# Performance work log

Hardware: AMD Instinct MI355X
Metric: run time of the kernel (lower is better)

The kernel has to match this reference:

```python
import jax, jax.numpy as jnp
import numpy as np
from jax import lax

B = 32; C_IN = 3; HW = 64
CL1_F = 64; CL1_K = 5
V = 1024
CL2_F = 128; CL2_K = 16
CL3_F = 256; CL3_K = 16
FC1_F = 512; FC2_F = 10
FC1_IN = CL3_F * (V // 16)  # 16384


def _sym_laplacian(k, v):
    # symmetric, spectral norm < 1 (mimics rescaled Laplacian 2L/lmax - I spectrum)
    a = jax.random.normal(k, (v, v), jnp.float32) / np.float32(np.sqrt(v))
    return (a + a.T) * jnp.float32(0.3)


def setup_inputs():
    key = jax.random.key(0)
    ks = jax.random.split(key, 10)
    def n(k, shape, s):
        return jax.random.normal(k, shape, jnp.float32) * jnp.float32(s)
    x = jax.random.normal(ks[0], (B, C_IN, HW, HW), jnp.float32)
    conv1_w = n(ks[1], (CL1_F, C_IN, CL1_K, CL1_K), 0.05)
    conv1_b = jnp.zeros((CL1_F,), jnp.float32)
    L1 = _sym_laplacian(ks[2], V)
    L2 = _sym_laplacian(ks[3], V // 4)
    g = HW // 2  # pooled grid side = 32
    ii, jj = jnp.meshgrid(jnp.arange(g), jnp.arange(g), indexing='ij')
    node_index = jnp.stack([ii.reshape(-1), jj.reshape(-1)], axis=1).astype(jnp.int32)  # [V,2]
    perm = jnp.arange(V, dtype=jnp.int32)
    k2_w = n(ks[4], (CL2_F, CL1_F * CL2_K), 0.04)
    k2_b = jnp.zeros((CL2_F,), jnp.float32)
    k3_w = n(ks[5], (CL3_F, CL2_F * CL3_K), 0.03)
    k3_b = jnp.zeros((CL3_F,), jnp.float32)
    fc1_w = n(ks[6], (FC1_F, FC1_IN), 0.01)
    fc1_b = jnp.zeros((FC1_F,), jnp.float32)
    fc2_w = n(ks[7], (FC2_F, FC1_F), 0.05)
    fc2_b = jnp.zeros((FC2_F,), jnp.float32)
    return {"x": x, "conv1_w": conv1_w, "conv1_b": conv1_b, "L1": L1, "L2": L2,
            "node_index": node_index, "perm": perm,
            "k2_w": k2_w, "k2_b": k2_b, "k3_w": k3_w, "k3_b": k3_b,
            "fc1_w": fc1_w, "fc1_b": fc1_b, "fc2_w": fc2_w, "fc2_b": fc2_b}


def _graph_conv(x, L, W, b, K):
    # x: (B, C, V). Chebyshev basis T_k(L) x, then linear over (C*K).
    Bb, C, Vv = x.shape
    x0 = jnp.transpose(x, (2, 1, 0)).reshape(Vv, C * Bb)  # [V, C*B]
    xs = [x0, L @ x0]
    for _ in range(K - 2):
        xs.append(2.0 * (L @ xs[-1]) - xs[-2])
    xk = jnp.stack(xs, axis=0).reshape(K, Vv, C, Bb)  # [K,V,C,B]
    xk = jnp.transpose(xk, (3, 1, 2, 0)).reshape(Bb * Vv, C * K)  # [B*V, C*K]
    out = xk @ W.T + b  # [B*V, Fout]
    return jnp.transpose(out.reshape(Bb, Vv, -1), (0, 2, 1))  # (B, Fout, V)


def reference(x, conv1_w, conv1_b, L1, L2, node_index, perm,
              k2_w, k2_b, k3_w, k3_b, fc1_w, fc1_b, fc2_w, fc2_b):
    pad = (CL1_K - 1) // 2
    y = lax.conv_general_dilated(x, conv1_w, (1, 1), [(pad, pad), (pad, pad)],
                                 dimension_numbers=('NCHW', 'OIHW', 'NCHW'))
    y = jax.nn.relu(y + conv1_b[None, :, None, None])
    Bb, C, H, Wd = y.shape
    y = y.reshape(Bb, C, H // 2, 2, Wd // 2, 2).max(axis=(3, 5))  # MaxPool2d(2,2)
    y = y[:, :, node_index[:, 0], node_index[:, 1]]  # (B, C, V)
    y = y[:, :, perm]
    # BatchNorm1d(affine=False), training-mode batch stats, biased variance
    mean = y.mean(axis=(0, 2), keepdims=True)
    var = y.var(axis=(0, 2), keepdims=True)
    y = (y - mean) * lax.rsqrt(var + 1e-5)
    y = jax.nn.relu(_graph_conv(y, L1, k2_w, k2_b, CL2_K))
    y = y.reshape(Bb, CL2_F, -1, 4).max(axis=-1)  # Graph_MaxPool(4)
    y = jax.nn.relu(_graph_conv(y, L2, k3_w, k3_b, CL3_K))
    y = y.reshape(Bb, CL3_F, -1, 4).max(axis=-1)
    y = y.reshape(Bb, FC1_IN)
    y = jax.nn.relu(y @ fc1_w.T + fc1_b)  # dropout p=0 -> identity
    return y @ fc2_w.T + fc2_b
```

## Files before the change

### kernel.cpp

```cpp
#include <hip/hip_runtime.h>
#include <hip/hip_bf16.h>

#define BB 32
#define C_IN 3
#define HW 64
#define V1 1024
#define CL2_F 128
#define V2 256
#define CL3_F 256
#define FC1_IN 16384

typedef unsigned short ushortT;
typedef __attribute__((ext_vector_type(8))) short bf16x8;
typedef __attribute__((ext_vector_type(8))) unsigned short u16x8;
typedef __attribute__((ext_vector_type(4))) float f32x4;

__device__ __forceinline__ float bfu2f(unsigned short u) {
  union { unsigned int i; float f; } x; x.i = ((unsigned)u) << 16; return x.f;
}
__device__ __forceinline__ unsigned short f2bf(float v) {
  union { float f; unsigned int i; } x; x.f = v;
  unsigned r = x.i + 0x7FFFu + ((x.i >> 16) & 1u);
  return (unsigned short)(r >> 16);
}
__device__ __forceinline__ void gload16(const ushortT* g, ushortT* l) {
  __builtin_amdgcn_global_load_lds((const __attribute__((address_space(1))) void*)g,
                                   (__attribute__((address_space(3))) void*)l, 16, 0, 0);
}

__global__ __launch_bounds__(256) void conv_pool_k(const float* __restrict__ x,
                                                   const float* __restrict__ w,
                                                   const float* __restrict__ bias,
                                                   float* __restrict__ P) {
  __shared__ float xs[3][7][72];
  __shared__ float wl[64][76];
  const int b = blockIdx.x >> 5, ph = blockIdx.x & 31;
  const int t = threadIdx.x;
  for (int i = t; i < 64 * 75; i += 256) wl[i / 75][i % 75] = w[i];
  for (int i = t; i < 3 * 7 * 72; i += 256) {
    int col = i % 72, rr = (i / 72) % 7, ci = i / (72 * 7);
    int ih = 2 * ph - 2 + rr, iw = col - 2;
    float v = 0.f;
    if (ih >= 0 && ih < HW && iw >= 0 && iw < HW)
      v = x[((b * 3 + ci) * HW + ih) * HW + iw];
    xs[ci][rr][col] = v;
  }
  __syncthreads();
  const int co = t >> 2, pq = t & 3;
  float acc[8][2][2];
#pragma unroll
  for (int i = 0; i < 8; ++i)
#pragma unroll
    for (int a = 0; a < 2; ++a)
#pragma unroll
      for (int d = 0; d < 2; ++d) acc[i][a][d] = 0.f;
  for (int ci = 0; ci < 3; ++ci) {
#pragma unroll
    for (int kh = 0; kh < 5; ++kh) {
      float w5[5];
#pragma unroll
      for (int j = 0; j < 5; ++j) w5[j] = wl[co][ci * 25 + kh * 5 + j];
#pragma unroll
      for (int dy = 0; dy < 2; ++dy) {
        const int r = kh + dy;
        float in[20];
#pragma unroll
        for (int q4 = 0; q4 < 5; ++q4) {
          float4 v4 = *(const float4*)&xs[ci][r][16 * pq + q4 * 4];
          in[q4 * 4 + 0] = v4.x; in[q4 * 4 + 1] = v4.y;
          in[q4 * 4 + 2] = v4.z; in[q4 * 4 + 3] = v4.w;
        }
#pragma unroll
        for (int i = 0; i < 8; ++i)
#pragma unroll
          for (int dx = 0; dx < 2; ++dx)
#pragma unroll
            for (int kw = 0; kw < 5; ++kw)
              acc[i][dy][dx] += w5[kw] * in[2 * i + dx + kw];
      }
    }
  }
  const float bv = bias[co];
#pragma unroll
  for (int i = 0; i < 8; ++i) {
    float m = fmaxf(fmaxf(acc[i][0][0], acc[i][0][1]), fmaxf(acc[i][1][0], acc[i][1][1]));
    P[((size_t)(b * 64 + co) << 10) + (ph << 5) + pq * 8 + i] = fmaxf(m + bv, 0.f);
  }
}

__global__ __launch_bounds__(256) void bn_part_k(const float* __restrict__ P,
                                                 float* __restrict__ buf) {
  int c = blockIdx.x, s = blockIdx.y;
  float s1 = 0.f, s2 = 0.f;
  for (int i = threadIdx.x; i < 4096; i += 256) {
    int b = s * 4 + (i >> 10), p = i & 1023;
    float v = P[((size_t)(b * 64 + c) << 10) + p];
    s1 += v; s2 += v * v;
  }
#pragma unroll
  for (int o = 32; o > 0; o >>= 1) { s1 += __shfl_down(s1, o); s2 += __shfl_down(s2, o); }
  __shared__ float sh[2][4];
  int wid = threadIdx.x >> 6;
  if ((threadIdx.x & 63) == 0) { sh[0][wid] = s1; sh[1][wid] = s2; }
  __syncthreads();
  if (threadIdx.x == 0) {
    buf[c * 8 + s] = sh[0][0] + sh[0][1] + sh[0][2] + sh[0][3];
    buf[512 + c * 8 + s] = sh[1][0] + sh[1][1] + sh[1][2] + sh[1][3];
  }
}
__global__ __launch_bounds__(64) void bn_comb_k(float* __restrict__ buf) {
  int c = threadIdx.x;
  float s1 = 0.f, s2 = 0.f;
#pragma unroll
  for (int s = 0; s < 8; ++s) { s1 += buf[c * 8 + s]; s2 += buf[512 + c * 8 + s]; }
  float mean = s1 / 32768.f;
  float var = s2 / 32768.f - mean * mean;
  buf[1024 + c] = mean;
  buf[1088 + c] = rsqrtf(var + 1e-5f);
}

__global__ __launch_bounds__(256) void build_x0_k(const float* __restrict__ P,
                                                  const float* __restrict__ buf,
                                                  const int* __restrict__ ni,
                                                  const int* __restrict__ perm,
                                                  ushortT* __restrict__ PGh,
                                                  ushortT* __restrict__ PGl,
                                                  ushortT* __restrict__ CW0) {
  __shared__ float vals[64][33];
  __shared__ int qv[32];
  const int b = blockIdx.x >> 5, vc = blockIdx.x & 31;
  const int t = threadIdx.x;
  if (t < 32) {
    int pv = perm[vc * 32 + t];
    qv[t] = ni[2 * pv] * 32 + ni[2 * pv + 1];
  }
  __syncthreads();
  {
    int c = t & 63, vh = t >> 6;
    float mean = buf[1024 + c], rstd = buf[1088 + c];
    const float* pc = &P[((size_t)(b * 64 + c)) << 10];
#pragma unroll
    for (int j = 0; j < 8; ++j) {
      int vl = vh * 8 + j;
      vals[c][vl] = (pc[qv[vl]] - mean) * rstd;
    }
  }
  __syncthreads();
  {
    int c = t & 63, vo = t >> 6;
    u16x8 h8, l8;
#pragma unroll
    for (int j = 0; j < 8; ++j) {
      float f = vals[c][vo * 8 + j];
      unsigned short h = f2bf(f);
      h8[j] = h; l8[j] = f2bf(f - bfu2f(h));
    }
    size_t base = ((size_t)(vc * 4 + vo) * 2048 + b * 64 + c) * 8;
    *(u16x8*)&PGh[base] = h8;
    *(u16x8*)&PGl[base] = l8;
  }
  {
    int co = t & 7, vl = t >> 3;
    u16x8 h8;
#pragma unroll
    for (int j = 0; j < 8; ++j) h8[j] = f2bf(vals[co * 8 + j][vl]);
    *(u16x8*)&CW0[((size_t)co * 32768 + b * 1024 + vc * 32 + vl) * 8] = h8;
  }
}

__global__ __launch_bounds__(256) void lsplit_k(const float* __restrict__ L,
                                                ushortT* __restrict__ Lh,
                                                ushortT* __restrict__ Ll, int V) {
  int id = blockIdx.x * 256 + threadIdx.x;
  int n = id & (V - 1), koct = id / V * 8;
  u16x8 h8, l8;
#pragma unroll
  for (int j = 0; j < 8; ++j) {
    float v = L[(size_t)(koct + j) * V + n];
    unsigned short h = f2bf(v);
    h8[j] = h; l8[j] = f2bf(v - bfu2f(h));
  }
  size_t o = (size_t)id * 8;
  *(u16x8*)&Lh[o] = h8;
  *(u16x8*)&Ll[o] = l8;
}

__global__ __launch_bounds__(256) void wprep_k(const float* __restrict__ W,
                                               ushortT* __restrict__ WAh,
                                               ushortT* __restrict__ WAl, int Cc, int Nf) {
  int d = blockIdx.x * 256 + threadIdx.x;
  if (d >= Nf * 16 * Cc) return;
  int c = d % Cc, kq = (d / Cc) % 16, f = d / (16 * Cc);
  float v = W[(size_t)f * (Cc * 16) + c * 16 + kq];
  unsigned short h = f2bf(v);
  WAh[d] = h; WAl[d] = f2bf(v - bfu2f(h));
}

template <int MODE, int SWZ>
__global__ __launch_bounds__(256, 2) void cheb_step_k(
    int Mld, int Kd, int mt,
    const ushortT* __restrict__ Ah, const ushortT* __restrict__ Al,
    const ushortT* __restrict__ Lbh, const ushortT* __restrict__ Lbl,
    ushortT* __restrict__ Ph, ushortT* __restrict__ Pl,
    ushortT* __restrict__ CW, int CB, int CSH) {
  __shared__ ushortT sA[2][2][8][520];
  __shared__ ushortT sB[2][2][8][520];
  int bx, by;
  if (SWZ) {
    const int id = blockIdx.x;
    const int xcd = id & 7, pos = id >> 3;
    bx = (xcd & 3) * 8 + (pos & 7);
    by = (xcd >> 2) * 8 + (pos >> 3);
  } else {
    bx = blockIdx.x % mt;
    by = blockIdx.x / mt;
  }
  const int m0 = bx * 64, n0 = by * 64;
  const int t = threadIdx.x, lane = t & 63;
  const int wr = (t >> 6) >> 1, wc = (t >> 6) & 1;
  const int lm = lane & 15, lq = lane >> 4;

  f32x4 acc[2][2];
#pragma unroll
  for (int mi = 0; mi < 2; ++mi)
#pragma unroll
    for (int nj = 0; nj < 2; ++nj) acc[mi][nj] = (f32x4){0.f, 0.f, 0.f, 0.f};

#define STAGEK(buf, k0)                                                            \
  {                                                                                \
    const int koct = (k0) >> 3;                                                    \
    _Pragma("unroll") for (int i = 0; i < 2; ++i) {                                \
      const int slot = (t + i * 256) >> 6;                                         \
      const int ln = t & 63;                                                       \
      const size_t ga = ((size_t)(koct + slot) * Mld + m0 + ln) * 8;               \
      const size_t gb = ((size_t)(koct + slot) * Kd + n0 + ln) * 8;                \
      gload16(Ah + ga, &sA[buf][0][slot][0]);                                      \
      gload16(Al + ga, &sA[buf][1][slot][0]);                                      \
      gload16(Lbh + gb, &sB[buf][0][slot][0]);                                     \
      gload16(Lbl + gb, &sB[buf][1][slot][0]);                                     \
    }                                                                              \
  }

  STAGEK(0, 0);
  __syncthreads();
  for (int k0 = 0; k0 < Kd; k0 += 64) {
    const int cur = (k0 >> 6) & 1;
    if (k0 + 64 < Kd) STAGEK(cur ^ 1, k0 + 64);
#pragma unroll
    for (int ks = 0; ks < 2; ++ks) {
      const int so = ks * 4 + lq;
      bf16x8 xah[2], xal[2], xbh[2], xbl[2];
#pragma unroll
      for (int mi = 0; mi < 2; ++mi) {
        const int r = (wr * 32 + mi * 16 + lm) * 8;
        xah[mi] = *(const bf16x8*)&sA[cur][0][so][r];
        xal[mi] = *(const bf16x8*)&sA[cur][1][so][r];
      }
#pragma unroll
      for (int nj = 0; nj < 2; ++nj) {
        const int r = (wc * 32 + nj * 16 + lm) * 8;
        xbh[nj] = *(const bf16x8*)&sB[cur][0][so][r];
        xbl[nj] = *(const bf16x8*)&sB[cur][1][so][r];
      }
#pragma unroll
      for (int mi = 0; mi < 2; ++mi)
#pragma unroll
        for (int nj = 0; nj < 2; ++nj) {
          acc[mi][nj] = __builtin_amdgcn_mfma_f32_16x16x32_bf16(xah[mi], xbh[nj], acc[mi][nj], 0, 0, 0);
          acc[mi][nj] = __builtin_amdgcn_mfma_f32_16x16x32_bf16(xal[mi], xbh[nj], acc[mi][nj], 0, 0, 0);
          acc[mi][nj] = __builtin_amdgcn_mfma_f32_16x16x32_bf16(xah[mi], xbl[nj], acc[mi][nj], 0, 0, 0);
        }
    }
    __syncthreads();
  }
#undef STAGEK

  float* fs = (float*)&sA[0][0][0][0];
#pragma unroll
  for (int mi = 0; mi < 2; ++mi)
#pragma unroll
    for (int nj = 0; nj < 2; ++nj)
#pragma unroll
      for (int j = 0; j < 4; ++j) {
        int gm_l = wr * 32 + mi * 16 + lq * 4 + j;
        int gn_l = wc * 32 + nj * 16 + lm;
        fs[gm_l * 65 + gn_l] = acc[mi][nj][j];
      }
  __syncthreads();

  const size_t noct0 = (size_t)(n0 >> 3);
#pragma unroll
  for (int r = 0; r < 2; ++r) {
    int id = t + r * 256;
    int gm_l = id >> 3, go = id & 7;
    size_t g = ((noct0 + go) * Mld + (m0 + gm_l)) * 8;
    float nv[8];
#pragma unroll
    for (int i = 0; i < 8; ++i) nv[i] = fs[gm_l * 65 + go * 8 + i];
    if (MODE == 1) {
      u16x8 ph = *(const u16x8*)&Ph[g];
      u16x8 pl = *(const u16x8*)&Pl[g];
#pragma unroll
      for (int i = 0; i < 8; ++i) nv[i] = 2.f * nv[i] - (bfu2f(ph[i]) + bfu2f(pl[i]));
    }
    u16x8 h8, l8;
#pragma unroll
    for (int i = 0; i < 8; ++i) {
      unsigned short h = f2bf(nv[i]);
      h8[i] = h; l8[i] = f2bf(nv[i] - bfu2f(h));
    }
    *(u16x8*)&Ph[g] = h8;
    *(u16x8*)&Pl[g] = l8;
    if (MODE == 1) {
#pragma unroll
      for (int i = 0; i < 8; ++i) fs[gm_l * 65 + go * 8 + i] = nv[i];
    }
  }
  __syncthreads();

  const int cBase = m0 & (CB - 1);
  const int bidx = m0 >> CSH;
  const size_t NNs = (size_t)Kd << 5;
#pragma unroll
  for (int r = 0; r < 2; ++r) {
    int id = t + r * 256;
    int gn_l = id & 63, coI = id >> 6;
    u16x8 h8;
#pragma unroll
    for (int i = 0; i < 8; ++i) h8[i] = f2bf(fs[(coI * 8 + i) * 65 + gn_l]);
    size_t cbase = ((size_t)((cBase >> 3) + coI) * NNs + (size_t)bidx * Kd + n0 + gn_l) * 8;
    *(u16x8*)&CW[cbase] = h8;
  }
}

template <int Cc>
__global__ __launch_bounds__(256) void wapply_k(
    int NN, int ldw,
    const ushortT* __restrict__ WAh, const ushortT* __restrict__ WAl,
    const ushortT* __restrict__ cwBase, size_t cwN,
    float* __restrict__ OUT) {
  constexpr int S = Cc / 2;
  const int m0 = blockIdx.x * 64, n0 = blockIdx.y * 128;
  const int t = threadIdx.x, lane = t & 63, wid = t >> 6;
  const int wr = wid >> 1, wc = wid & 1;
  const int lm = lane & 15, lq = lane >> 4;

  const size_t wBase = (size_t)(m0 + wr * 32 + lm) * ldw + lq * 8;
  const int nb = n0 + wc * 64 + lm;

  f32x4 acc[2][4];
#pragma unroll
  for (int mi = 0; mi < 2; ++mi)
#pragma unroll
    for (int nj = 0; nj < 4; ++nj) acc[mi][nj] = (f32x4){0.f, 0.f, 0.f, 0.f};

#pragma unroll 4
  for (int s = 0; s < S; ++s) {
    const int buf = (Cc == 64) ? (s >> 1) : (s >> 2);
    const int lo = (Cc == 64) ? ((s & 1) * 4) : ((s & 3) * 4);
    const ushortT* xb = cwBase + (size_t)buf * cwN;
    bf16x8 wh[2], wl[2], xf[4];
#pragma unroll
    for (int mi = 0; mi < 2; ++mi) {
      size_t o = wBase + (size_t)s * 32 + (size_t)mi * 16 * ldw;
      wh[mi] = *(const bf16x8*)(WAh + o);
      wl[mi] = *(const bf16x8*)(WAl + o);
    }
#pragma unroll
    for (int nj = 0; nj < 4; ++nj)
      xf[nj] = *(const bf16x8*)(xb + ((size_t)(lo + lq) * NN + nb + nj * 16) * 8);
#pragma unroll
    for (int mi = 0; mi < 2; ++mi)
#pragma unroll
      for (int nj = 0; nj < 4; ++nj) {
        acc[mi][nj] = __builtin_amdgcn_mfma_f32_16x16x32_bf16(wh[mi], xf[nj], acc[mi][nj], 0, 0, 0);
        acc[mi][nj] = __builtin_amdgcn_mfma_f32_16x16x32_bf16(wl[mi], xf[nj], acc[mi][nj], 0, 0, 0);
      }
  }

#pragma unroll
  for (int mi = 0; mi < 2; ++mi)
#pragma unroll
    for (int nj = 0; nj < 4; ++nj)
#pragma unroll
      for (int j = 0; j < 4; ++j) {
        int gm = m0 + wr * 32 + mi * 16 + lq * 4 + j;
        int gn = n0 + wc * 64 + nj * 16 + lm;
        OUT[(size_t)gm * NN + gn] = acc[mi][nj][j];
      }
}

__global__ __launch_bounds__(256) void relu_pool1_k(const float* __restrict__ OUT1T,
                                                    const float* __restrict__ b2,
                                                    ushortT* __restrict__ PG2h,
                                                    ushortT* __restrict__ PG2l,
                                                    ushortT* __restrict__ CW0) {
  __shared__ float sval[128][9];
  const int b = blockIdx.x >> 5, vc = blockIdx.x & 31;
  const int t = threadIdx.x;
  {
    int f = t & 127, h = t >> 7;
    float bb = b2[f];
    const float* src = &OUT1T[(size_t)f * 32768 + b * 1024 + vc * 32];
#pragma unroll
    for (int i = 0; i < 4; ++i) {
      int v2l = h * 4 + i;
      float4 r = *(const float4*)&src[v2l * 4];
      float m = fmaxf(fmaxf(r.x, r.y), fmaxf(r.z, r.w));
      sval[f][v2l] = fmaxf(m + bb, 0.f);
    }
  }
  __syncthreads();
  if (t < 128) {
    int f = t;
    u16x8 h8, l8;
#pragma unroll
    for (int j = 0; j < 8; ++j) {
      float v = sval[f][j];
      unsigned short h = f2bf(v);
      h8[j] = h; l8[j] = f2bf(v - bfu2f(h));
    }
    size_t base = ((size_t)vc * 4096 + b * 128 + f) * 8;
    *(u16x8*)&PG2h[base] = h8;
    *(u16x8*)&PG2l[base] = l8;
  } else {
    int q = t - 128;
    int co = q & 15, v2l = q >> 4;
    u16x8 h8;
#pragma unroll
    for (int j = 0; j < 8; ++j) h8[j] = f2bf(sval[co * 8 + j][v2l]);
    *(u16x8*)&CW0[((size_t)co * 8192 + b * 256 + vc * 8 + v2l) * 8] = h8;
  }
}

__global__ __launch_bounds__(256) void relu_pool2_k(const float* __restrict__ OUT2T,
                                                    const float* __restrict__ b3,
                                                    float* __restrict__ At) {
  int n = blockIdx.x * 256 + threadIdx.x;
  int v3 = n & 63, f = (n >> 6) & 255, b = n >> 14;
  float4 r = *(const float4*)&OUT2T[((size_t)f * 32 + b) * 256 + v3 * 4];
  float m = fmaxf(fmaxf(r.x, r.y), fmaxf(r.z, r.w));
  At[(size_t)b * FC1_IN + f * 64 + v3] = fmaxf(m + b3[f], 0.f);
}

__global__ __launch_bounds__(256) void fc1_part_k(const float* __restrict__ At,
                                                  const float* __restrict__ W1,
                                                  float* __restrict__ part) {
  __shared__ float sWt[64][68];
  __shared__ float sA[64][33];
  const int jt = blockIdx.x, ks = blockIdx.y;
  const int j0 = jt * 64, kb = ks * 512;
  const int t = threadIdx.x;
  const int b = t & 31, jg = t >> 5;
  float acc[8] = {};
  for (int k0 = kb; k0 < kb + 512; k0 += 64) {
    __syncthreads();
    {
      int jr = t >> 2, kq = t & 3;
      const float* wp = &W1[(size_t)(j0 + jr) * FC1_IN + k0 + kq * 16];
#pragma unroll
      for (int i = 0; i < 4; ++i) {
        float4 w4 = *(const float4*)(wp + 4 * i);
        int kk = kq * 16 + 4 * i;
        sWt[kk + 0][jr] = w4.x; sWt[kk + 1][jr] = w4.y;
        sWt[kk + 2][jr] = w4.z; sWt[kk + 3][jr] = w4.w;
      }
    }
    {
      int br = t >> 3, ko = t & 7;
      const float* ap = &At[(size_t)br * FC1_IN + k0 + ko * 8];
      float4 a0 = *(const float4*)ap;
      float4 a1 = *(const float4*)(ap + 4);
      int kk = ko * 8;
      sA[kk + 0][br] = a0.x; sA[kk + 1][br] = a0.y; sA[kk + 2][br] = a0.z; sA[kk + 3][br] = a0.w;
      sA[kk + 4][br] = a1.x; sA[kk + 5][br] = a1.y; sA[kk + 6][br] = a1.z; sA[kk + 7][br] = a1.w;
    }
    __syncthreads();
#pragma unroll 8
    for (int kk = 0; kk < 64; ++kk) {
      float a = sA[kk][b];
      float wv[8];
      *(float4*)wv = *(const float4*)&sWt[kk][jg * 8];
      *(float4*)(wv + 4) = *(const float4*)&sWt[kk][jg * 8 + 4];
#pragma unroll
      for (int i = 0; i < 8; ++i) acc[i] += wv[i] * a;
    }
  }
#pragma unroll
  for (int i = 0; i < 8; ++i)
    part[((size_t)ks * 512 + j0 + jg * 8 + i) * 32 + b] = acc[i];
}

__global__ __launch_bounds__(256) void fc1_combine_k(const float* __restrict__ part,
                                                     const float* __restrict__ b1,
                                                     float* __restrict__ h) {
  int n = blockIdx.x * 256 + threadIdx.x;
  int b = n >> 9, j = n & 511;
  float s = b1[j];
#pragma unroll
  for (int ks = 0; ks < 32; ++ks) s += part[((size_t)ks * 512 + j) * 32 + b];
  h[n] = fmaxf(s, 0.f);
}

__global__ __launch_bounds__(64) void fc2_k(const float* __restrict__ h,
                                            const float* __restrict__ W2,
                                            const float* __restrict__ b2f,
                                            float* __restrict__ out) {
  int n = blockIdx.x * 64 + threadIdx.x;
  if (n >= 320) return;
  int b = n / 10, o = n % 10;
  float s = b2f[o];
  const float* hp = h + b * 512;
  const float* wp = W2 + o * 512;
  for (int j = 0; j < 512; ++j) s += hp[j] * wp[j];
  out[n] = s;
}

extern "C" void kernel_launch(void* const* d_in, const int* in_sizes, int n_in,
                              void* d_out, int out_size, void* d_ws, size_t ws_size,
                              hipStream_t stream) {
  const float* x      = (const float*)d_in[0];
  const float* conv1w = (const float*)d_in[1];
  const float* conv1b = (const float*)d_in[2];
  const float* L1     = (const float*)d_in[3];
  const float* L2     = (const float*)d_in[4];
  const int*   ni     = (const int*)d_in[5];
  const int*   perm   = (const int*)d_in[6];
  const float* k2w    = (const float*)d_in[7];
  const float* k2b    = (const float*)d_in[8];
  const float* k3w    = (const float*)d_in[9];
  const float* k3b    = (const float*)d_in[10];
  const float* fc1w   = (const float*)d_in[11];
  const float* fc1b   = (const float*)d_in[12];
  const float* fc2w   = (const float*)d_in[13];
  const float* fc2b   = (const float*)d_in[14];
  float* out = (float*)d_out;

  char* ws = (char*)d_ws;
  const size_t MB = 1024 * 1024;
  float*   P    = (float*)(ws + 0);
  ushortT* cw1  = (ushortT*)(ws + 8 * MB);
  const size_t CW1N = 2u * 1024 * 1024;
  ushortT* pgAh = (ushortT*)(ws + 72 * MB);
  ushortT* pgAl = (ushortT*)(ws + 76 * MB);
  ushortT* pgBh = (ushortT*)(ws + 80 * MB);
  ushortT* pgBl = (ushortT*)(ws + 84 * MB);
  float*   OUT1T = (float*)(ws + 88 * MB);
  ushortT* L1h  = (ushortT*)(ws + 105 * MB);
  ushortT* L1l  = (ushortT*)(ws + 107 * MB);
  ushortT* WA1h = (ushortT*)(ws + 109 * MB);
  ushortT* WA1l = (ushortT*)(ws + 109 * MB + 262144);
  float*   BNB  = (float*)(ws + 110 * MB);
  ushortT* cw2  = (ushortT*)(ws + 0);
  const size_t CW2N = 1024u * 1024;
  ushortT* pg2Ah = (ushortT*)(ws + 32 * MB);
  ushortT* pg2Al = (ushortT*)(ws + 34 * MB);
  ushortT* pg2Bh = (ushortT*)(ws + 36 * MB);
  ushortT* pg2Bl = (ushortT*)(ws + 38 * MB);
  float*   OUT2T = (float*)(ws + 40 * MB);
  ushortT* L2h  = (ushortT*)(ws + 48 * MB);
  ushortT* L2l  = (ushortT*)(ws + 48 * MB + 131072);
  ushortT* WA2h = (ushortT*)(ws + 49 * MB);
  ushortT* WA2l = (ushortT*)(ws + 50 * MB);
  float*   At   = (float*)(ws + 51 * MB);
  float*   PART = (float*)(ws + 53 * MB);
  float*   H    = (float*)(ws + 55 * MB);

  conv_pool_k<<<1024, 256, 0, stream>>>(x, conv1w, conv1b, P);
  bn_part_k<<<dim3(64, 8), 256, 0, stream>>>(P, BNB);
  bn_comb_k<<<1, 64, 0, stream>>>(BNB);
  lsplit_k<<<512, 256, 0, stream>>>(L1, L1h, L1l, 1024);
  wprep_k<<<512, 256, 0, stream>>>(k2w, WA1h, WA1l, 64, 128);
  build_x0_k<<<1024, 256, 0, stream>>>(P, BNB, ni, perm, pgAh, pgAl, cw1 + 0 * CW1N);

  cheb_step_k<0, 1><<<512, 256, 0, stream>>>(2048, 1024, 32, pgAh, pgAl, L1h, L1l,
                                             pgBh, pgBl, cw1 + 1 * CW1N, 64, 6);
  for (int k = 2; k < 16; ++k) {
    ushortT *ah, *al, *oh, *ol;
    if (k & 1) { ah = pgAh; al = pgAl; oh = pgBh; ol = pgBl; }
    else       { ah = pgBh; al = pgBl; oh = pgAh; ol = pgAl; }
    cheb_step_k<1, 1><<<512, 256, 0, stream>>>(2048, 1024, 32, ah, al, L1h, L1l,
                                               oh, ol, cw1 + (size_t)k * CW1N, 64, 6);
  }
  wapply_k<64><<<dim3(2, 256), 256, 0, stream>>>(32768, 1024, WA1h, WA1l, cw1, CW1N, OUT1T);

  relu_pool1_k<<<1024, 256, 0, stream>>>(OUT1T, k2b, pg2Ah, pg2Al, cw2 + 0 * CW2N);
  lsplit_k<<<32, 256, 0, stream>>>(L2, L2h, L2l, 256);
  wprep_k<<<2048, 256, 0, stream>>>(k3w, WA2h, WA2l, 128, 256);

  cheb_step_k<0, 0><<<256, 256, 0, stream>>>(4096, 256, 64, pg2Ah, pg2Al, L2h, L2l,
                                             pg2Bh, pg2Bl, cw2 + 1 * CW2N, 128, 7);
  for (int k = 2; k < 16; ++k) {
    ushortT *ah, *al, *oh, *ol;
    if (k & 1) { ah = pg2Ah; al = pg2Al; oh = pg2Bh; ol = pg2Bl; }
    else       { ah = pg2Bh; al = pg2Bl; oh = pg2Ah; ol = pg2Al; }
    cheb_step_k<1, 0><<<256, 256, 0, stream>>>(4096, 256, 64, ah, al, L2h, L2l,
                                               oh, ol, cw2 + (size_t)k * CW2N, 128, 7);
  }
  wapply_k<128><<<dim3(4, 64), 256, 0, stream>>>(8192, 2048, WA2h, WA2l, cw2, CW2N, OUT2T);

  relu_pool2_k<<<2048, 256, 0, stream>>>(OUT2T, k3b, At);
  fc1_part_k<<<dim3(8, 32), 256, 0, stream>>>(At, fc1w, PART);
  fc1_combine_k<<<64, 256, 0, stream>>>(PART, fc1b, H);
  fc2_k<<<5, 64, 0, stream>>>(H, fc2w, fc2b, out);
}
```

Before: 606.4 us.

## Split-K the weight-apply GEMMs and read Laplacian operands directly from global

The weight-apply kernels now split their reduction dimension across a grid z-dimension, 2 slices for stage 1 and 4 for stage 2. Each slice writes its own partial output buffer, and the relu/pool kernels sum the partials before the max. This raises the block count to fill more CUs, at the cost of extra partial-buffer traffic and a relocated workspace layout. Separately, the Chebyshev step kernel no longer stages the Laplacian tile in LDS. Each wave loads its B fragments straight from global into registers, halving shared memory but relying on cache hits for reuse across waves.

```diff
diff --git a/kernel.cpp b/kernel.cpp
--- a/kernel.cpp
+++ b/kernel.cpp
@@ -204,7 +204,6 @@
     ushortT* __restrict__ Ph, ushortT* __restrict__ Pl,
     ushortT* __restrict__ CW, int CB, int CSH) {
   __shared__ ushortT sA[2][2][8][520];
-  __shared__ ushortT sB[2][2][8][520];
   int bx, by;
   if (SWZ) {
     const int id = blockIdx.x;
@@ -219,6 +218,7 @@
   const int t = threadIdx.x, lane = t & 63;
   const int wr = (t >> 6) >> 1, wc = (t >> 6) & 1;
   const int lm = lane & 15, lq = lane >> 4;
+  const size_t bCol = (size_t)(n0 + wc * 32 + lm);
 
   f32x4 acc[2][2];
 #pragma unroll
@@ -226,30 +226,36 @@
 #pragma unroll
     for (int nj = 0; nj < 2; ++nj) acc[mi][nj] = (f32x4){0.f, 0.f, 0.f, 0.f};
 
-#define STAGEK(buf, k0)                                                            \
+#define STAGEA(buf, k0)                                                            \
   {                                                                                \
     const int koct = (k0) >> 3;                                                    \
     _Pragma("unroll") for (int i = 0; i < 2; ++i) {                                \
       const int slot = (t + i * 256) >> 6;                                         \
       const int ln = t & 63;                                                       \
       const size_t ga = ((size_t)(koct + slot) * Mld + m0 + ln) * 8;               \
-      const size_t gb = ((size_t)(koct + slot) * Kd + n0 + ln) * 8;                \
       gload16(Ah + ga, &sA[buf][0][slot][0]);                                      \
       gload16(Al + ga, &sA[buf][1][slot][0]);                                      \
-      gload16(Lbh + gb, &sB[buf][0][slot][0]);                                     \
-      gload16(Lbl + gb, &sB[buf][1][slot][0]);                                     \
     }                                                                              \
   }
 
-  STAGEK(0, 0);
+  STAGEA(0, 0);
   __syncthreads();
   for (int k0 = 0; k0 < Kd; k0 += 64) {
     const int cur = (k0 >> 6) & 1;
-    if (k0 + 64 < Kd) STAGEK(cur ^ 1, k0 + 64);
+    if (k0 + 64 < Kd) STAGEA(cur ^ 1, k0 + 64);
+    bf16x8 xbh[2][2], xbl[2][2];
+#pragma unroll
+    for (int ks = 0; ks < 2; ++ks)
+#pragma unroll
+      for (int nj = 0; nj < 2; ++nj) {
+        size_t o = ((size_t)((k0 >> 3) + ks * 4 + lq) * Kd + bCol + nj * 16) * 8;
+        xbh[ks][nj] = *(const bf16x8*)(Lbh + o);
+        xbl[ks][nj] = *(const bf16x8*)(Lbl + o);
+      }
 #pragma unroll
     for (int ks = 0; ks < 2; ++ks) {
       const int so = ks * 4 + lq;
-      bf16x8 xah[2], xal[2], xbh[2], xbl[2];
+      bf16x8 xah[2], xal[2];
 #pragma unroll
       for (int mi = 0; mi < 2; ++mi) {
         const int r = (wr * 32 + mi * 16 + lm) * 8;
@@ -257,23 +263,17 @@
         xal[mi] = *(const bf16x8*)&sA[cur][1][so][r];
       }
 #pragma unroll
-      for (int nj = 0; nj < 2; ++nj) {
-        const int r = (wc * 32 + nj * 16 + lm) * 8;
-        xbh[nj] = *(const bf16x8*)&sB[cur][0][so][r];
-        xbl[nj] = *(const bf16x8*)&sB[cur][1][so][r];
-      }
-#pragma unroll
       for (int mi = 0; mi < 2; ++mi)
 #pragma unroll
         for (int nj = 0; nj < 2; ++nj) {
-          acc[mi][nj] = __builtin_amdgcn_mfma_f32_16x16x32_bf16(xah[mi], xbh[nj], acc[mi][nj], 0, 0, 0);
-          acc[mi][nj] = __builtin_amdgcn_mfma_f32_16x16x32_bf16(xal[mi], xbh[nj], acc[mi][nj], 0, 0, 0);
-          acc[mi][nj] = __builtin_amdgcn_mfma_f32_16x16x32_bf16(xah[mi], xbl[nj], acc[mi][nj], 0, 0, 0);
+          acc[mi][nj] = __builtin_amdgcn_mfma_f32_16x16x32_bf16(xah[mi], xbh[ks][nj], acc[mi][nj], 0, 0, 0);
+          acc[mi][nj] = __builtin_amdgcn_mfma_f32_16x16x32_bf16(xal[mi], xbh[ks][nj], acc[mi][nj], 0, 0, 0);
+          acc[mi][nj] = __builtin_amdgcn_mfma_f32_16x16x32_bf16(xah[mi], xbl[ks][nj], acc[mi][nj], 0, 0, 0);
         }
     }
     __syncthreads();
   }
-#undef STAGEK
+#undef STAGEA
 
   float* fs = (float*)&sA[0][0][0][0];
 #pragma unroll
@@ -333,13 +333,16 @@
   }
 }
 
-template <int Cc>
+template <int Cc, int NSPL>
 __global__ __launch_bounds__(256) void wapply_k(
     int NN, int ldw,
     const ushortT* __restrict__ WAh, const ushortT* __restrict__ WAl,
     const ushortT* __restrict__ cwBase, size_t cwN,
-    float* __restrict__ OUT) {
+    float* __restrict__ OUT, size_t outStride) {
   constexpr int S = Cc / 2;
+  constexpr int SPZ = S / NSPL;
+  const int z = blockIdx.z;
+  OUT += (size_t)z * outStride;
   const int m0 = blockIdx.x * 64, n0 = blockIdx.y * 128;
   const int t = threadIdx.x, lane = t & 63, wid = t >> 6;
   const int wr = wid >> 1, wc = wid & 1;
@@ -354,8 +357,8 @@
 #pragma unroll
     for (int nj = 0; nj < 4; ++nj) acc[mi][nj] = (f32x4){0.f, 0.f, 0.f, 0.f};
 
-#pragma unroll 4
-  for (int s = 0; s < S; ++s) {
+#pragma unroll 8
+  for (int s = z * SPZ; s < (z + 1) * SPZ; ++s) {
     const int buf = (Cc == 64) ? (s >> 1) : (s >> 2);
     const int lo = (Cc == 64) ? ((s & 1) * 4) : ((s & 3) * 4);
     const ushortT* xb = cwBase + (size_t)buf * cwN;
@@ -390,7 +393,7 @@
       }
 }
 
-__global__ __launch_bounds__(256) void relu_pool1_k(const float* __restrict__ OUT1T,
+__global__ __launch_bounds__(256) void relu_pool1_k(const float* __restrict__ OUT1P,
                                                     const float* __restrict__ b2,
                                                     ushortT* __restrict__ PG2h,
                                                     ushortT* __restrict__ PG2l,
@@ -398,15 +401,18 @@
   __shared__ float sval[128][9];
   const int b = blockIdx.x >> 5, vc = blockIdx.x & 31;
   const int t = threadIdx.x;
+  const size_t PS = (size_t)128 * 32768;
   {
     int f = t & 127, h = t >> 7;
     float bb = b2[f];
-    const float* src = &OUT1T[(size_t)f * 32768 + b * 1024 + vc * 32];
+    const float* src = &OUT1P[(size_t)f * 32768 + b * 1024 + vc * 32];
 #pragma unroll
     for (int i = 0; i < 4; ++i) {
       int v2l = h * 4 + i;
-      float4 r = *(const float4*)&src[v2l * 4];
-      float m = fmaxf(fmaxf(r.x, r.y), fmaxf(r.z, r.w));
+      float4 r0 = *(const float4*)&src[v2l * 4];
+      float4 r1 = *(const float4*)&src[PS + v2l * 4];
+      float s0 = r0.x + r1.x, s1 = r0.y + r1.y, s2 = r0.z + r1.z, s3 = r0.w + r1.w;
+      float m = fmaxf(fmaxf(s0, s1), fmaxf(s2, s3));
       sval[f][v2l] = fmaxf(m + bb, 0.f);
     }
   }
@@ -433,13 +439,22 @@
   }
 }
 
-__global__ __launch_bounds__(256) void relu_pool2_k(const float* __restrict__ OUT2T,
+__global__ __launch_bounds__(256) void relu_pool2_k(const float* __restrict__ OUT2P,
                                                     const float* __restrict__ b3,
                                                     float* __restrict__ At) {
   int n = blockIdx.x * 256 + threadIdx.x;
   int v3 = n & 63, f = (n >> 6) & 255, b = n >> 14;
-  float4 r = *(const float4*)&OUT2T[((size_t)f * 32 + b) * 256 + v3 * 4];
-  float m = fmaxf(fmaxf(r.x, r.y), fmaxf(r.z, r.w));
+  const size_t PS = (size_t)256 * 8192;
+  size_t base = ((size_t)f * 32 + b) * 256 + v3 * 4;
+  float4 r0 = *(const float4*)&OUT2P[base];
+  float4 r1 = *(const float4*)&OUT2P[PS + base];
+  float4 r2 = *(const float4*)&OUT2P[2 * PS + base];
+  float4 r3 = *(const float4*)&OUT2P[3 * PS + base];
+  float s0 = r0.x + r1.x + r2.x + r3.x;
+  float s1 = r0.y + r1.y + r2.y + r3.y;
+  float s2 = r0.z + r1.z + r2.z + r3.z;
+  float s3 = r0.w + r1.w + r2.w + r3.w;
+  float m = fmaxf(fmaxf(s0, s1), fmaxf(s2, s3));
   At[(size_t)b * FC1_IN + f * 64 + v3] = fmaxf(m + b3[f], 0.f);
 }
 
@@ -545,26 +560,26 @@
   ushortT* pgAl = (ushortT*)(ws + 76 * MB);
   ushortT* pgBh = (ushortT*)(ws + 80 * MB);
   ushortT* pgBl = (ushortT*)(ws + 84 * MB);
-  float*   OUT1T = (float*)(ws + 88 * MB);
-  ushortT* L1h  = (ushortT*)(ws + 105 * MB);
-  ushortT* L1l  = (ushortT*)(ws + 107 * MB);
-  ushortT* WA1h = (ushortT*)(ws + 109 * MB);
-  ushortT* WA1l = (ushortT*)(ws + 109 * MB + 262144);
-  float*   BNB  = (float*)(ws + 110 * MB);
+  float*   OUT1P = (float*)(ws + 88 * MB);
+  ushortT* L1h  = (ushortT*)(ws + 121 * MB);
+  ushortT* L1l  = (ushortT*)(ws + 123 * MB);
+  ushortT* WA1h = (ushortT*)(ws + 125 * MB);
+  ushortT* WA1l = (ushortT*)(ws + 125 * MB + 262144);
+  float*   BNB  = (float*)(ws + 126 * MB);
   ushortT* cw2  = (ushortT*)(ws + 0);
   const size_t CW2N = 1024u * 1024;
   ushortT* pg2Ah = (ushortT*)(ws + 32 * MB);
   ushortT* pg2Al = (ushortT*)(ws + 34 * MB);
   ushortT* pg2Bh = (ushortT*)(ws + 36 * MB);
   ushortT* pg2Bl = (ushortT*)(ws + 38 * MB);
-  float*   OUT2T = (float*)(ws + 40 * MB);
-  ushortT* L2h  = (ushortT*)(ws + 48 * MB);
-  ushortT* L2l  = (ushortT*)(ws + 48 * MB + 131072);
-  ushortT* WA2h = (ushortT*)(ws + 49 * MB);
-  ushortT* WA2l = (ushortT*)(ws + 50 * MB);
-  float*   At   = (float*)(ws + 51 * MB);
-  float*   PART = (float*)(ws + 53 * MB);
-  float*   H    = (float*)(ws + 55 * MB);
+  float*   OUT2P = (float*)(ws + 40 * MB);
+  ushortT* L2h  = (ushortT*)(ws + 73 * MB);
+  ushortT* L2l  = (ushortT*)(ws + 73 * MB + 131072);
+  ushortT* WA2h = (ushortT*)(ws + 74 * MB);
+  ushortT* WA2l = (ushortT*)(ws + 75 * MB);
+  float*   At   = (float*)(ws + 76 * MB);
+  float*   PART = (float*)(ws + 78 * MB);
+  float*   H    = (float*)(ws + 80 * MB);
 
   conv_pool_k<<<1024, 256, 0, stream>>>(x, conv1w, conv1b, P);
   bn_part_k<<<dim3(64, 8), 256, 0, stream>>>(P, BNB);
@@ -582,9 +597,10 @@
     cheb_step_k<1, 1><<<512, 256, 0, stream>>>(2048, 1024, 32, ah, al, L1h, L1l,
                                                oh, ol, cw1 + (size_t)k * CW1N, 64, 6);
   }
-  wapply_k<64><<<dim3(2, 256), 256, 0, stream>>>(32768, 1024, WA1h, WA1l, cw1, CW1N, OUT1T);
-
-  relu_pool1_k<<<1024, 256, 0, stream>>>(OUT1T, k2b, pg2Ah, pg2Al, cw2 + 0 * CW2N);
+  wapply_k<64, 2><<<dim3(2, 256, 2), 256, 0, stream>>>(32768, 1024, WA1h, WA1l,
+                                                       cw1, CW1N, OUT1P, (size_t)128 * 32768);
+
+  relu_pool1_k<<<1024, 256, 0, stream>>>(OUT1P, k2b, pg2Ah, pg2Al, cw2 + 0 * CW2N);
   lsplit_k<<<32, 256, 0, stream>>>(L2, L2h, L2l, 256);
   wprep_k<<<2048, 256, 0, stream>>>(k3w, WA2h, WA2l, 128, 256);
 
@@ -597,9 +613,10 @@
     cheb_step_k<1, 0><<<256, 256, 0, stream>>>(4096, 256, 64, ah, al, L2h, L2l,
                                                oh, ol, cw2 + (size_t)k * CW2N, 128, 7);
   }
-  wapply_k<128><<<dim3(4, 64), 256, 0, stream>>>(8192, 2048, WA2h, WA2l, cw2, CW2N, OUT2T);
-
-  relu_pool2_k<<<2048, 256, 0, stream>>>(OUT2T, k3b, At);
+  wapply_k<128, 4><<<dim3(4, 64, 4), 256, 0, stream>>>(8192, 2048, WA2h, WA2l,
+                                                       cw2, CW2N, OUT2P, (size_t)256 * 8192);
+
+  relu_pool2_k<<<2048, 256, 0, stream>>>(OUT2P, k3b, At);
   fc1_part_k<<<dim3(8, 32), 256, 0, stream>>>(At, fc1w, PART);
   fc1_combine_k<<<64, 256, 0, stream>>>(PART, fc1b, H);
   fc2_k<<<5, 64, 0, stream>>>(H, fc2w, fc2b, out);
```

Result: slower. 648.2 us (+6.9%).
